# Kernel optimization log

Measured on AMD Instinct MI355X. Metric: run time of the kernel, lower is better.

## Reference

```python
import jax, jax.numpy as jnp
import numpy as np

B, S, D = 4, 2048, 1024
H = 2 * D          # hidden_dim = 2*n_embd
A = H // 16        # adapt_dim
E = 8              # num_experts
GS = 4             # group_size
G = E // GS        # num_groups
K = 2              # top-k experts within group


def _ln(x, g, b, eps=1e-5):
    m = x.mean(-1, keepdims=True)
    v = ((x - m) ** 2).mean(-1, keepdims=True)
    return (x - m) * jax.lax.rsqrt(v + eps) * g + b


def setup_inputs() -> dict:
    key = jax.random.key(0)
    ks = jax.random.split(key, 14)
    n = lambda k, shape, s: jax.random.normal(k, shape, jnp.float32) * s
    sc = 1.0 / float(np.sqrt(D))
    asc = 0.01 / float(np.sqrt(A))
    return {
        'x': n(ks[0], (B, S, D), 1.0),
        'Wu': n(ks[1], (H, D), sc),        # shared_up
        'Wg': n(ks[2], (H, D), sc),        # shared_gate
        'Wd': n(ks[3], (D, H), sc),        # shared_down
        'Wpre': n(ks[4], (A, D), sc * 0.01),   # pre_adapt
        'Wpost': n(ks[5], (A, H), sc * 0.01),  # post_adapt
        'ln_g': jnp.ones((A,), jnp.float32),
        'ln_b': jnp.zeros((A,), jnp.float32),
        'Wap': n(ks[6], (H, A), sc * 0.01),    # adapt_proj
        'Wea': n(ks[7], (E, A, A), asc),       # per-expert adapter linears
        'ln_eg': jnp.ones((E, A), jnp.float32),
        'ln_eb': jnp.zeros((E, A), jnp.float32),
        'Wep': n(ks[8], (H, A), asc),          # expert_proj
        'Wop': n(ks[9], (D, H), asc),          # output_proj
        'Wgr': n(ks[10], (G, D), 0.001),       # router_group
        'Wer': n(ks[11], (GS, D), 0.001),      # router_expert
    }


def _forward(x, Wu, Wg, Wd, Wpre, Wpost, ln_g, ln_b, Wap, Wea, ln_eg, ln_eb, Wep, Wop, Wgr, Wer):
    N = B * S
    xf = x.reshape(N, D)
    # --- hierarchical router ---
    gl = xf @ Wgr.T                              # [N,G]
    gp = jax.nn.softmax(gl, axis=-1)
    gw, gi = jax.lax.top_k(gp, 1)                # top-1 group
    el = xf @ Wer.T                              # [N,GS]
    ep = jax.nn.softmax(el, axis=-1)
    lw, li = jax.lax.top_k(ep, K)                # top-k local experts
    lw = lw / (lw.sum(-1, keepdims=True) + 1e-7)
    fw = gw * lw                                 # [N,K] final weights
    idx = gi * GS + li                           # [N,K] global expert ids (distinct per token)
    dispatch = jnp.zeros((N, E), x.dtype).at[jnp.arange(N)[:, None], idx].set(fw)
    load = dispatch.sum(0)
    target = load.sum() / E
    rloss = 0.001 * (jnp.mean((load - target) ** 2) + jnp.mean(gl ** 2) + jnp.mean(el ** 2))
    # --- shared expert MLP ---
    hidden = jax.nn.silu(x @ Wg.T) * (x @ Wu.T)  # [B,S,H]
    ai = _ln(x @ Wpre.T, ln_g, ln_b)             # [B,S,A]
    ao = _ln(hidden @ Wpost.T, ln_g, ln_b)       # [B,S,A]
    aw = jax.nn.silu(jnp.clip(jnp.einsum('bsa,bta->bst', ai, ao), -5.0, 5.0))  # [B,S,S]
    adapt = jnp.einsum('bst,bta->bsa', aw, ai) @ Wap.T
    hidden = hidden + 0.1 * adapt
    shared = hidden @ Wd.T                       # [B,S,D]
    # --- expert group (dense form of masked gather/scatter; w==0 off-mask) ---
    w = dispatch.reshape(B, S, E)
    h0 = x @ Wpre.T                              # [B,S,A]
    he = _ln(jnp.einsum('bsa,eca->bsec', h0, Wea), ln_eg, ln_eb)  # [B,S,E,A]
    M = Wop @ Wep                                # output_proj o expert_proj, [D,A]
    out = shared * w.sum(-1, keepdims=True) + 0.1 * jnp.einsum('bsec,bse,dc->bsd', he, w, M)
    return out, rloss


def reference(x, Wu, Wg, Wd, Wpre, Wpost, ln_g, ln_b, Wap, Wea, ln_eg, ln_eb, Wep, Wop, Wgr, Wer):
    return _forward(x, Wu, Wg, Wd, Wpre, Wpost, ln_g, ln_b, Wap, Wea, ln_eg, ln_eb, Wep, Wop, Wgr, Wer)
```

## Files before the change

### kernel.cpp

```cpp
#include <hip/hip_runtime.h>
#include <math.h>


typedef __bf16 bf16_t;
typedef __attribute__((ext_vector_type(8))) __bf16 bf16x8;
typedef __attribute__((ext_vector_type(4))) float f32x4;

__device__ __forceinline__ float b2f(bf16_t v) { return (float)v; }
__device__ __forceinline__ bf16_t f2b(float v) { return (bf16_t)v; }
__device__ __forceinline__ float siluf(float v) { return v / (1.f + expf(-v)); }

static constexpr int Bb = 4, S = 2048, D = 1024, H = 2048, A = 128, E = 8;
static constexpr int N = Bb * S;

typedef __attribute__((address_space(1))) void gvoid;
typedef __attribute__((address_space(3))) void svoid;
__device__ __forceinline__ void gll16(const bf16_t* g, bf16_t* l) {
  __builtin_amdgcn_global_load_lds((gvoid*)g, (svoid*)l, 16, 0, 0);
}

__device__ __forceinline__ long tidx(int row, int k, int K, int lgTR) {
  int TRm = (1 << lgTR) - 1;
  int q = (k >> 3) & 3;
  int p = q ^ ((row >> 1) & 3);
  return ((((long)(row >> lgTR) * (K >> 5) + (k >> 5)) << lgTR) + (row & TRm)) * 32 +
         ((long)p << 3);
}

__device__ __forceinline__ bf16x8 ld8f(const float* p) {
  float4 a = *reinterpret_cast<const float4*>(p);
  float4 b = *reinterpret_cast<const float4*>(p + 4);
  bf16x8 r;
  r[0] = f2b(a.x); r[1] = f2b(a.y); r[2] = f2b(a.z); r[3] = f2b(a.w);
  r[4] = f2b(b.x); r[5] = f2b(b.y); r[6] = f2b(b.z); r[7] = f2b(b.w);
  return r;
}
__device__ __forceinline__ void split8(const float* p, bf16x8& h, bf16x8& l) {
  float4 a = *reinterpret_cast<const float4*>(p);
  float4 b = *reinterpret_cast<const float4*>(p + 4);
  float v[8] = {a.x, a.y, a.z, a.w, b.x, b.y, b.z, b.w};
#pragma unroll
  for (int j = 0; j < 8; j++) {
    bf16_t hh = f2b(v[j]);
    h[j] = hh;
    l[j] = f2b(v[j] - b2f(hh));
  }
}
__device__ __forceinline__ bf16x8 ld8m(const void* p, int row, int k, int K, int m) {
  if (m == 1) return ld8f(reinterpret_cast<const float*>(p) + (long)row * K + k);
  if (m == 2)
    return *reinterpret_cast<const bf16x8*>(
        reinterpret_cast<const bf16_t*>(p) + tidx(row, k, K, 7));
  return *reinterpret_cast<const bf16x8*>(
      reinterpret_cast<const bf16_t*>(p) + (long)row * K + k);
}

template <int LGTR, int LGNKS>
__global__ __launch_bounds__(256) void split_tiled(
    const float* __restrict__ in, bf16_t* __restrict__ hi,
    bf16_t* __restrict__ lo, long total, int K) {
  long stride = (long)gridDim.x * 256;
  for (long o = (long)blockIdx.x * 256 + threadIdx.x; o < total; o += stride) {
    int p = (int)(o & 3);
    long t = o >> 2;
    int r = (int)(t & ((1 << LGTR) - 1));
    long t2 = t >> LGTR;
    int ks = (int)(t2 & ((1 << LGNKS) - 1));
    long rt = t2 >> LGNKS;
    long row = (rt << LGTR) + r;
    int k = (ks << 5) + ((p ^ ((r >> 1) & 3)) << 3);
    bf16x8 h, l;
    split8(in + row * K + k, h, l);
    reinterpret_cast<bf16x8*>(hi)[o] = h;
    reinterpret_cast<bf16x8*>(lo)[o] = l;
  }
}

template <int WM, int WN, int MODE>
__global__ __launch_bounds__(256) void gemm_nt_b(
    const void* __restrict__ Ag, const void* __restrict__ Bg,
    void* __restrict__ Cv, int M, int Nn, int K,
    const float* __restrict__ aux, int aF, int bF) {
  constexpr int BM = 2 * WM, BN = 2 * WN, AM = WM / 16, AN = WN / 16;
  constexpr int LDT = 40;
  __shared__ alignas(16) bf16_t As[BM * LDT];
  __shared__ alignas(16) bf16_t Bs[BN * LDT];

  const int tid = threadIdx.x;
  const int wave = tid >> 6, lane = tid & 63;
  const int wr = wave >> 1, wc = wave & 1;
  const int quad = lane >> 4, l16 = lane & 15;
  const int rowA0 = blockIdx.y * BM, rowB0 = blockIdx.x * BN;

  f32x4 acc[AM][AN] = {};

  for (int k0 = 0; k0 < K; k0 += 32) {
    for (int c = tid; c < BM * 4; c += 256) {
      int r = c >> 2, kc = c & 3;
      *reinterpret_cast<bf16x8*>(&As[r * LDT + kc * 8]) =
          ld8m(Ag, rowA0 + r, k0 + kc * 8, K, aF);
    }
    for (int c = tid; c < BN * 4; c += 256) {
      int r = c >> 2, kc = c & 3;
      *reinterpret_cast<bf16x8*>(&Bs[r * LDT + kc * 8]) =
          ld8m(Bg, rowB0 + r, k0 + kc * 8, K, bF);
    }
    __syncthreads();
    bf16x8 af[AM], bfv[AN];
#pragma unroll
    for (int i = 0; i < AM; i++)
      af[i] = *reinterpret_cast<bf16x8*>(&As[(wr * WM + i * 16 + l16) * LDT + quad * 8]);
#pragma unroll
    for (int j = 0; j < AN; j++)
      bfv[j] = *reinterpret_cast<bf16x8*>(&Bs[(wc * WN + j * 16 + l16) * LDT + quad * 8]);
#pragma unroll
    for (int i = 0; i < AM; i++)
#pragma unroll
      for (int j = 0; j < AN; j++)
        acc[i][j] = __builtin_amdgcn_mfma_f32_16x16x32_bf16(af[i], bfv[j], acc[i][j], 0, 0, 0);
    __syncthreads();
  }

#pragma unroll
  for (int i = 0; i < AM; i++)
#pragma unroll
    for (int j = 0; j < AN; j++)
#pragma unroll
      for (int r = 0; r < 4; r++) {
        int row = rowA0 + wr * WM + i * 16 + quad * 4 + r;
        int col = rowB0 + wc * WN + j * 16 + l16;
        long o = (long)row * Nn + col;
        float v = acc[i][j][r];
        if constexpr (MODE == 0) {
          reinterpret_cast<bf16_t*>(Cv)[o] = f2b(v);
        } else if constexpr (MODE == 1) {
          v = fminf(fmaxf(v, -5.f), 5.f);
          reinterpret_cast<bf16_t*>(Cv)[o] = f2b(siluf(v));
        } else if constexpr (MODE == 2) {
          float* C = reinterpret_cast<float*>(Cv);
          C[o] = C[o] + 0.1f * v;
        } else {
          float* C = reinterpret_cast<float*>(Cv);
          C[o] = C[o] * aux[row] + 0.1f * v;
        }
      }
}

__global__ __launch_bounds__(256) void gemm_gu_g(
    const bf16_t* __restrict__ xhT, const bf16_t* __restrict__ xlT,
    const bf16_t* __restrict__ WghT, const bf16_t* __restrict__ WglT,
    const bf16_t* __restrict__ WuhT, const bf16_t* __restrict__ WulT,
    bf16_t* __restrict__ Hh, bf16_t* __restrict__ Hl) {
  __shared__ alignas(16) bf16_t Ah[128 * 32];
  __shared__ alignas(16) bf16_t Al[128 * 32];
  __shared__ alignas(16) bf16_t B1h[64 * 32];
  __shared__ alignas(16) bf16_t B1l[64 * 32];
  __shared__ alignas(16) bf16_t B2h[64 * 32];
  __shared__ alignas(16) bf16_t B2l[64 * 32];

  const int tid = threadIdx.x;
  const int wave = tid >> 6, lane = tid & 63;
  const int wr = wave >> 1, wc = wave & 1;
  const int quad = lane >> 4, l16 = lane & 15;
  const int sw = (quad ^ ((l16 >> 1) & 3)) << 3;
  const int bm = blockIdx.y, bn = blockIdx.x;
  constexpr int nks = D / 32;
  const int wo = wave << 9;

  f32x4 ag[4][2] = {}, au[4][2] = {};

  for (int ks = 0; ks < nks; ks++) {
    long ao = (((long)bm * nks + ks) << 12) + wo + lane * 8;
    long bo = (((long)bn * nks + ks) << 11) + wo + lane * 8;
    gll16(xhT + ao, Ah + wo);
    gll16(xhT + ao + 2048, Ah + wo + 2048);
    gll16(xlT + ao, Al + wo);
    gll16(xlT + ao + 2048, Al + wo + 2048);
    gll16(WghT + bo, B1h + wo);
    gll16(WglT + bo, B1l + wo);
    gll16(WuhT + bo, B2h + wo);
    gll16(WulT + bo, B2l + wo);
    __syncthreads();
    bf16x8 afh[4], afl[4], b1h[2], b1l[2], b2h[2], b2l[2];
#pragma unroll
    for (int i = 0; i < 4; i++) {
      int ro = (wr * 64 + i * 16 + l16) * 32 + sw;
      afh[i] = *reinterpret_cast<bf16x8*>(&Ah[ro]);
      afl[i] = *reinterpret_cast<bf16x8*>(&Al[ro]);
    }
#pragma unroll
    for (int j = 0; j < 2; j++) {
      int ro = (wc * 32 + j * 16 + l16) * 32 + sw;
      b1h[j] = *reinterpret_cast<bf16x8*>(&B1h[ro]);
      b1l[j] = *reinterpret_cast<bf16x8*>(&B1l[ro]);
      b2h[j] = *reinterpret_cast<bf16x8*>(&B2h[ro]);
      b2l[j] = *reinterpret_cast<bf16x8*>(&B2l[ro]);
    }
#pragma unroll
    for (int i = 0; i < 4; i++)
#pragma unroll
      for (int j = 0; j < 2; j++) {
        ag[i][j] = __builtin_amdgcn_mfma_f32_16x16x32_bf16(afh[i], b1h[j], ag[i][j], 0, 0, 0);
        ag[i][j] = __builtin_amdgcn_mfma_f32_16x16x32_bf16(afh[i], b1l[j], ag[i][j], 0, 0, 0);
        ag[i][j] = __builtin_amdgcn_mfma_f32_16x16x32_bf16(afl[i], b1h[j], ag[i][j], 0, 0, 0);
        au[i][j] = __builtin_amdgcn_mfma_f32_16x16x32_bf16(afh[i], b2h[j], au[i][j], 0, 0, 0);
        au[i][j] = __builtin_amdgcn_mfma_f32_16x16x32_bf16(afh[i], b2l[j], au[i][j], 0, 0, 0);
        au[i][j] = __builtin_amdgcn_mfma_f32_16x16x32_bf16(afl[i], b2h[j], au[i][j], 0, 0, 0);
      }
    __syncthreads();
  }

#pragma unroll
  for (int i = 0; i < 4; i++)
#pragma unroll
    for (int j = 0; j < 2; j++)
#pragma unroll
      for (int r = 0; r < 4; r++) {
        int row = bm * 128 + wr * 64 + i * 16 + quad * 4 + r;
        int col = bn * 64 + wc * 32 + j * 16 + l16;
        long o = tidx(row, col, H, 7) + (col & 7);
        float v = siluf(ag[i][j][r]) * au[i][j][r];
        bf16_t hh = f2b(v);
        Hh[o] = hh;
        Hl[o] = f2b(v - b2f(hh));
      }
}

__global__ __launch_bounds__(256) void gemm_dn_g(
    const bf16_t* __restrict__ HhT, const bf16_t* __restrict__ HlT,
    const bf16_t* __restrict__ WdhT, const bf16_t* __restrict__ WdlT,
    float* __restrict__ Cg) {
  __shared__ alignas(16) bf16_t Ah[128 * 32];
  __shared__ alignas(16) bf16_t Al[128 * 32];
  __shared__ alignas(16) bf16_t Bh[128 * 32];
  __shared__ alignas(16) bf16_t Bl[128 * 32];

  const int tid = threadIdx.x;
  const int wave = tid >> 6, lane = tid & 63;
  const int wr = wave >> 1, wc = wave & 1;
  const int quad = lane >> 4, l16 = lane & 15;
  const int sw = (quad ^ ((l16 >> 1) & 3)) << 3;
  const int by = blockIdx.y, bx = blockIdx.x;
  constexpr int nks = H / 32;
  const int wo = wave << 9;

  f32x4 acc[4][4] = {};

  for (int ks = 0; ks < nks; ks++) {
    long ao = (((long)by * nks + ks) << 12) + wo + lane * 8;
    long bo = (((long)bx * nks + ks) << 12) + wo + lane * 8;
    gll16(HhT + ao, Ah + wo);
    gll16(HhT + ao + 2048, Ah + wo + 2048);
    gll16(HlT + ao, Al + wo);
    gll16(HlT + ao + 2048, Al + wo + 2048);
    gll16(WdhT + bo, Bh + wo);
    gll16(WdhT + bo + 2048, Bh + wo + 2048);
    gll16(WdlT + bo, Bl + wo);
    gll16(WdlT + bo + 2048, Bl + wo + 2048);
    __syncthreads();
    bf16x8 afh[4], afl[4], bfh[4], bfl[4];
#pragma unroll
    for (int i = 0; i < 4; i++) {
      int ro = (wr * 64 + i * 16 + l16) * 32 + sw;
      afh[i] = *reinterpret_cast<bf16x8*>(&Ah[ro]);
      afl[i] = *reinterpret_cast<bf16x8*>(&Al[ro]);
    }
#pragma unroll
    for (int j = 0; j < 4; j++) {
      int ro = (wc * 64 + j * 16 + l16) * 32 + sw;
      bfh[j] = *reinterpret_cast<bf16x8*>(&Bh[ro]);
      bfl[j] = *reinterpret_cast<bf16x8*>(&Bl[ro]);
    }
#pragma unroll
    for (int i = 0; i < 4; i++)
#pragma unroll
      for (int j = 0; j < 4; j++) {
        acc[i][j] = __builtin_amdgcn_mfma_f32_16x16x32_bf16(afh[i], bfh[j], acc[i][j], 0, 0, 0);
        acc[i][j] = __builtin_amdgcn_mfma_f32_16x16x32_bf16(afh[i], bfl[j], acc[i][j], 0, 0, 0);
        acc[i][j] = __builtin_amdgcn_mfma_f32_16x16x32_bf16(afl[i], bfh[j], acc[i][j], 0, 0, 0);
      }
    __syncthreads();
  }

#pragma unroll
  for (int i = 0; i < 4; i++)
#pragma unroll
    for (int j = 0; j < 4; j++)
#pragma unroll
      for (int r = 0; r < 4; r++) {
        int row = by * 128 + wr * 64 + i * 16 + quad * 4 + r;
        int col = bx * 128 + wc * 64 + j * 16 + l16;
        Cg[(long)row * D + col] = acc[i][j][r];
      }
}

__global__ __launch_bounds__(256) void fused_adapt(
    const bf16_t* __restrict__ aib, const bf16_t* __restrict__ aob,
    const bf16_t* __restrict__ aiT, bf16_t* __restrict__ outp,
    int oLd, int oOff, const float* __restrict__ wsum) {
  constexpr int LDQ = 136;
  constexpr int LDP = 72;
  __shared__ alignas(16) bf16_t Qs[64 * LDQ];
  __shared__ alignas(16) bf16_t Os[64 * LDQ];
  __shared__ alignas(16) bf16_t Ps[64 * LDP];
  __shared__ alignas(16) bf16_t Vs[128 * LDP];

  const int tid = threadIdx.x;
  const int wave = tid >> 6, lane = tid & 63;
  const int wr = wave >> 1, wc = wave & 1;
  const int quad = lane >> 4, l16 = lane & 15;
  const int b = blockIdx.y;
  const int q0 = blockIdx.x * 64;

  for (int c = tid; c < 1024; c += 256) {
    int r = c >> 4, cc = c & 15;
    *reinterpret_cast<bf16x8*>(&Qs[r * LDQ + cc * 8]) =
        *reinterpret_cast<const bf16x8*>(&aib[((long)b * S + q0 + r) * A + cc * 8]);
  }

  f32x4 o[2][4] = {};

  for (int tt = 0; tt < S / 64; tt++) {
    const int t0 = tt * 64;
    __syncthreads();
    for (int c = tid; c < 1024; c += 256) {
      int r = c >> 4, cc = c & 15;
      *reinterpret_cast<bf16x8*>(&Os[r * LDQ + cc * 8]) =
          *reinterpret_cast<const bf16x8*>(&aob[((long)b * S + t0 + r) * A + cc * 8]);
    }
    for (int c = tid; c < 1024; c += 256) {
      int r = c >> 3, cc = c & 7;
      *reinterpret_cast<bf16x8*>(&Vs[r * LDP + cc * 8]) =
          *reinterpret_cast<const bf16x8*>(&aiT[((long)b * A + r) * S + t0 + cc * 8]);
    }
    __syncthreads();
    f32x4 p[2][2] = {};
#pragma unroll
    for (int ks = 0; ks < 4; ks++) {
      bf16x8 af[2], bfv[2];
#pragma unroll
      for (int i = 0; i < 2; i++)
        af[i] = *reinterpret_cast<bf16x8*>(&Qs[(wr * 32 + i * 16 + l16) * LDQ + ks * 32 + quad * 8]);
#pragma unroll
      for (int j = 0; j < 2; j++)
        bfv[j] = *reinterpret_cast<bf16x8*>(&Os[(wc * 32 + j * 16 + l16) * LDQ + ks * 32 + quad * 8]);
#pragma unroll
      for (int i = 0; i < 2; i++)
#pragma unroll
        for (int j = 0; j < 2; j++)
          p[i][j] = __builtin_amdgcn_mfma_f32_16x16x32_bf16(af[i], bfv[j], p[i][j], 0, 0, 0);
    }
#pragma unroll
    for (int i = 0; i < 2; i++)
#pragma unroll
      for (int j = 0; j < 2; j++)
#pragma unroll
        for (int r = 0; r < 4; r++) {
          int row = wr * 32 + i * 16 + quad * 4 + r;
          int col = wc * 32 + j * 16 + l16;
          float v = fminf(fmaxf(p[i][j][r], -5.f), 5.f);
          Ps[row * LDP + col] = f2b(siluf(v));
        }
    __syncthreads();
#pragma unroll
    for (int ks = 0; ks < 2; ks++) {
      bf16x8 paf[2], vbf[4];
#pragma unroll
      for (int i = 0; i < 2; i++)
        paf[i] = *reinterpret_cast<bf16x8*>(&Ps[(wr * 32 + i * 16 + l16) * LDP + ks * 32 + quad * 8]);
#pragma unroll
      for (int j = 0; j < 4; j++)
        vbf[j] = *reinterpret_cast<bf16x8*>(&Vs[(wc * 64 + j * 16 + l16) * LDP + ks * 32 + quad * 8]);
#pragma unroll
      for (int i = 0; i < 2; i++)
#pragma unroll
        for (int j = 0; j < 4; j++)
          o[i][j] = __builtin_amdgcn_mfma_f32_16x16x32_bf16(paf[i], vbf[j], o[i][j], 0, 0, 0);
    }
  }

#pragma unroll
  for (int i = 0; i < 2; i++)
#pragma unroll
    for (int j = 0; j < 4; j++)
#pragma unroll
      for (int r = 0; r < 4; r++) {
        int row = q0 + wr * 32 + i * 16 + quad * 4 + r;
        int col = wc * 64 + j * 16 + l16;
        long token = (long)b * S + row;
        float sc = wsum ? wsum[token] : 1.f;
        outp[token * oLd + oOff + col] = f2b(o[i][j][r] * sc);
      }
}

__global__ __launch_bounds__(256) void gemm_mb_splitk(
    const float* __restrict__ Ag, const bf16_t* __restrict__ Bg,
    float* __restrict__ Mp, int M, int Nn, int K) {
  constexpr int BM = 64, BN = 64, LDT = 40;
  __shared__ alignas(16) bf16_t As[BM * LDT];
  __shared__ alignas(16) bf16_t Bs[BN * LDT];
  const int tid = threadIdx.x;
  const int wave = tid >> 6, lane = tid & 63;
  const int wr = wave >> 1, wc = wave & 1;
  const int quad = lane >> 4, l16 = lane & 15;
  const int rowA0 = blockIdx.y * BM, rowB0 = blockIdx.x * BN;
  const int kz = blockIdx.z;
  const int ks0 = kz * (K / 8), ks1 = ks0 + K / 8;

  f32x4 acc[2][2] = {};
  for (int k0 = ks0; k0 < ks1; k0 += 32) {
    for (int c = tid; c < BM * 4; c += 256) {
      int r = c >> 2, kc = c & 3;
      *reinterpret_cast<bf16x8*>(&As[r * LDT + kc * 8]) =
          ld8f(Ag + (long)(rowA0 + r) * K + k0 + kc * 8);
    }
    for (int c = tid; c < BN * 4; c += 256) {
      int r = c >> 2, kc = c & 3;
      *reinterpret_cast<bf16x8*>(&Bs[r * LDT + kc * 8]) =
          *reinterpret_cast<const bf16x8*>(&Bg[(long)(rowB0 + r) * K + k0 + kc * 8]);
    }
    __syncthreads();
    bf16x8 af[2], bfv[2];
#pragma unroll
    for (int i = 0; i < 2; i++)
      af[i] = *reinterpret_cast<bf16x8*>(&As[(wr * 32 + i * 16 + l16) * LDT + quad * 8]);
#pragma unroll
    for (int j = 0; j < 2; j++)
      bfv[j] = *reinterpret_cast<bf16x8*>(&Bs[(wc * 32 + j * 16 + l16) * LDT + quad * 8]);
#pragma unroll
    for (int i = 0; i < 2; i++)
#pragma unroll
      for (int j = 0; j < 2; j++)
        acc[i][j] = __builtin_amdgcn_mfma_f32_16x16x32_bf16(af[i], bfv[j], acc[i][j], 0, 0, 0);
    __syncthreads();
  }
#pragma unroll
  for (int i = 0; i < 2; i++)
#pragma unroll
    for (int j = 0; j < 2; j++)
#pragma unroll
      for (int r = 0; r < 4; r++) {
        int row = rowA0 + wr * 32 + i * 16 + quad * 4 + r;
        int col = rowB0 + wc * 32 + j * 16 + l16;
        Mp[(long)kz * M * Nn + (long)row * Nn + col] = acc[i][j][r];
      }
}

__global__ __launch_bounds__(256) void mb_combine(
    const float* __restrict__ Mp, bf16_t* __restrict__ outp, int total,
    int ld, int coff) {
  int i = blockIdx.x * 256 + threadIdx.x;
  if (i >= total) return;
  float s = 0.f;
#pragma unroll
  for (int z = 0; z < 8; z++) s += Mp[(long)z * total + i];
  outp[(long)(i >> 7) * ld + coff + (i & 127)] = f2b(s);
}

__global__ __launch_bounds__(256) void gemm_dn_hl(
    const float* __restrict__ Ag, const float* __restrict__ Bg,
    float* __restrict__ Cg, int M, int Nn, int K) {
  constexpr int BM = 128, BN = 128, LDT = 40;
  __shared__ alignas(16) bf16_t Ah[BM * LDT];
  __shared__ alignas(16) bf16_t Al[BM * LDT];
  __shared__ alignas(16) bf16_t Bh[BN * LDT];
  __shared__ alignas(16) bf16_t Bl[BN * LDT];

  const int tid = threadIdx.x;
  const int wave = tid >> 6, lane = tid & 63;
  const int wr = wave >> 1, wc = wave & 1;
  const int quad = lane >> 4, l16 = lane & 15;
  const int rowA0 = blockIdx.y * BM, rowB0 = blockIdx.x * BN;

  f32x4 acc[4][4] = {};

  for (int k0 = 0; k0 < K; k0 += 32) {
    for (int c = tid; c < BM * 4; c += 256) {
      int r = c >> 2, kc = c & 3;
      bf16x8 h, l;
      split8(&Ag[(long)(rowA0 + r) * K + k0 + kc * 8], h, l);
      *reinterpret_cast<bf16x8*>(&Ah[r * LDT + kc * 8]) = h;
      *reinterpret_cast<bf16x8*>(&Al[r * LDT + kc * 8]) = l;
    }
    for (int c = tid; c < BN * 4; c += 256) {
      int r = c >> 2, kc = c & 3;
      bf16x8 h, l;
      split8(&Bg[(long)(rowB0 + r) * K + k0 + kc * 8], h, l);
      *reinterpret_cast<bf16x8*>(&Bh[r * LDT + kc * 8]) = h;
      *reinterpret_cast<bf16x8*>(&Bl[r * LDT + kc * 8]) = l;
    }
    __syncthreads();
    bf16x8 afh[4], afl[4], bfh[4], bfl[4];
#pragma unroll
    for (int i = 0; i < 4; i++) {
      int ro = (wr * 64 + i * 16 + l16) * LDT + quad * 8;
      afh[i] = *reinterpret_cast<bf16x8*>(&Ah[ro]);
      afl[i] = *reinterpret_cast<bf16x8*>(&Al[ro]);
    }
#pragma unroll
    for (int j = 0; j < 4; j++) {
      int ro = (wc * 64 + j * 16 + l16) * LDT + quad * 8;
      bfh[j] = *reinterpret_cast<bf16x8*>(&Bh[ro]);
      bfl[j] = *reinterpret_cast<bf16x8*>(&Bl[ro]);
    }
#pragma unroll
    for (int i = 0; i < 4; i++)
#pragma unroll
      for (int j = 0; j < 4; j++) {
        acc[i][j] = __builtin_amdgcn_mfma_f32_16x16x32_bf16(afh[i], bfh[j], acc[i][j], 0, 0, 0);
        acc[i][j] = __builtin_amdgcn_mfma_f32_16x16x32_bf16(afh[i], bfl[j], acc[i][j], 0, 0, 0);
        acc[i][j] = __builtin_amdgcn_mfma_f32_16x16x32_bf16(afl[i], bfh[j], acc[i][j], 0, 0, 0);
      }
    __syncthreads();
  }

#pragma unroll
  for (int i = 0; i < 4; i++)
#pragma unroll
    for (int j = 0; j < 4; j++)
#pragma unroll
      for (int r = 0; r < 4; r++) {
        int row = rowA0 + wr * 64 + i * 16 + quad * 4 + r;
        int col = rowB0 + wc * 64 + j * 16 + l16;
        Cg[(long)row * Nn + col] = acc[i][j][r];
      }
}

__global__ __launch_bounds__(256) void gemm_gu_hl(
    const float* __restrict__ x, const float* __restrict__ Wg,
    const float* __restrict__ Wu, float* __restrict__ Cg, int M, int Nn, int K) {
  constexpr int BM = 128, BN = 64, LDT = 40;
  __shared__ alignas(16) bf16_t Ah[BM * LDT];
  __shared__ alignas(16) bf16_t Al[BM * LDT];
  __shared__ alignas(16) bf16_t B1h[BN * LDT];
  __shared__ alignas(16) bf16_t B1l[BN * LDT];
  __shared__ alignas(16) bf16_t B2h[BN * LDT];
  __shared__ alignas(16) bf16_t B2l[BN * LDT];

  const int tid = threadIdx.x;
  const int wave = tid >> 6, lane = tid & 63;
  const int wr = wave >> 1, wc = wave & 1;
  const int quad = lane >> 4, l16 = lane & 15;
  const int rowA0 = blockIdx.y * BM, rowB0 = blockIdx.x * BN;

  f32x4 ag[4][2] = {}, au[4][2] = {};

  for (int k0 = 0; k0 < K; k0 += 32) {
    for (int c = tid; c < BM * 4; c += 256) {
      int r = c >> 2, kc = c & 3;
      bf16x8 h, l;
      split8(&x[(long)(rowA0 + r) * K + k0 + kc * 8], h, l);
      *reinterpret_cast<bf16x8*>(&Ah[r * LDT + kc * 8]) = h;
      *reinterpret_cast<bf16x8*>(&Al[r * LDT + kc * 8]) = l;
    }
    for (int c = tid; c < BN * 4; c += 256) {
      int r = c >> 2, kc = c & 3;
      long idx = (long)(rowB0 + r) * K + k0 + kc * 8;
      bf16x8 h, l;
      split8(&Wg[idx], h, l);
      *reinterpret_cast<bf16x8*>(&B1h[r * LDT + kc * 8]) = h;
      *reinterpret_cast<bf16x8*>(&B1l[r * LDT + kc * 8]) = l;
      split8(&Wu[idx], h, l);
      *reinterpret_cast<bf16x8*>(&B2h[r * LDT + kc * 8]) = h;
      *reinterpret_cast<bf16x8*>(&B2l[r * LDT + kc * 8]) = l;
    }
    __syncthreads();
    bf16x8 afh[4], afl[4], b1h[2], b1l[2], b2h[2], b2l[2];
#pragma unroll
    for (int i = 0; i < 4; i++) {
      int ro = (wr * 64 + i * 16 + l16) * LDT + quad * 8;
      afh[i] = *reinterpret_cast<bf16x8*>(&Ah[ro]);
      afl[i] = *reinterpret_cast<bf16x8*>(&Al[ro]);
    }
#pragma unroll
    for (int j = 0; j < 2; j++) {
      int ro = (wc * 32 + j * 16 + l16) * LDT + quad * 8;
      b1h[j] = *reinterpret_cast<bf16x8*>(&B1h[ro]);
      b1l[j] = *reinterpret_cast<bf16x8*>(&B1l[ro]);
      b2h[j] = *reinterpret_cast<bf16x8*>(&B2h[ro]);
      b2l[j] = *reinterpret_cast<bf16x8*>(&B2l[ro]);
    }
#pragma unroll
    for (int i = 0; i < 4; i++)
#pragma unroll
      for (int j = 0; j < 2; j++) {
        ag[i][j] = __builtin_amdgcn_mfma_f32_16x16x32_bf16(afh[i], b1h[j], ag[i][j], 0, 0, 0);
        ag[i][j] = __builtin_amdgcn_mfma_f32_16x16x32_bf16(afh[i], b1l[j], ag[i][j], 0, 0, 0);
        ag[i][j] = __builtin_amdgcn_mfma_f32_16x16x32_bf16(afl[i], b1h[j], ag[i][j], 0, 0, 0);
        au[i][j] = __builtin_amdgcn_mfma_f32_16x16x32_bf16(afh[i], b2h[j], au[i][j], 0, 0, 0);
        au[i][j] = __builtin_amdgcn_mfma_f32_16x16x32_bf16(afh[i], b2l[j], au[i][j], 0, 0, 0);
        au[i][j] = __builtin_amdgcn_mfma_f32_16x16x32_bf16(afl[i], b2h[j], au[i][j], 0, 0, 0);
      }
    __syncthreads();
  }

#pragma unroll
  for (int i = 0; i < 4; i++)
#pragma unroll
    for (int j = 0; j < 2; j++)
#pragma unroll
      for (int r = 0; r < 4; r++) {
        int row = rowA0 + wr * 64 + i * 16 + quad * 4 + r;
        int col = rowB0 + wc * 32 + j * 16 + l16;
        Cg[(long)row * Nn + col] = siluf(ag[i][j][r]) * au[i][j][r];
      }
}

__global__ __launch_bounds__(256) void router_kernel(
    const float* __restrict__ x, const float* __restrict__ Wgr,
    const float* __restrict__ Wer, int* __restrict__ eidx,
    float* __restrict__ fw, float* __restrict__ wsum,
    float* __restrict__ lpart) {
  __shared__ float part[4][12];
  const int wv = threadIdx.x >> 6;
  const int lane = threadIdx.x & 63;
  const int token = blockIdx.x * 4 + wv;
  if (lane < 12) part[wv][lane] = 0.f;
  const float* xp = x + (long)token * D;
  float xr[16];
#pragma unroll
  for (int i = 0; i < 16; i++) xr[i] = xp[lane + i * 64];
  float dots[6];
#pragma unroll
  for (int w = 0; w < 6; w++) {
    const float* wp = (w < 2) ? (Wgr + (long)w * D) : (Wer + (long)(w - 2) * D);
    float s = 0.f;
#pragma unroll
    for (int i = 0; i < 16; i++) s += xr[i] * wp[lane + i * 64];
#pragma unroll
    for (int off = 32; off; off >>= 1) s += __shfl_xor(s, off);
    dots[w] = s;
  }
  if (lane == 0) {
    float gl0 = dots[0], gl1 = dots[1];
    float mg = fmaxf(gl0, gl1);
    float e0 = expf(gl0 - mg), e1 = expf(gl1 - mg);
    float inv = 1.f / (e0 + e1);
    float gp0 = e0 * inv, gp1 = e1 * inv;
    int gi = (gp1 > gp0) ? 1 : 0;
    float gw = gi ? gp1 : gp0;
    float el[4] = {dots[2], dots[3], dots[4], dots[5]};
    float me = fmaxf(fmaxf(el[0], el[1]), fmaxf(el[2], el[3]));
    float ep[4], es = 0.f;
#pragma unroll
    for (int j = 0; j < 4; j++) { ep[j] = expf(el[j] - me); es += ep[j]; }
    float inve = 1.f / es;
#pragma unroll
    for (int j = 0; j < 4; j++) ep[j] *= inve;
    int i1 = 0;
    for (int j = 1; j < 4; j++) if (ep[j] > ep[i1]) i1 = j;
    int i2 = (i1 == 0) ? 1 : 0;
    for (int j = 0; j < 4; j++) if (j != i1 && j != i2 && ep[j] > ep[i2]) i2 = j;
    float l1 = ep[i1], l2 = ep[i2];
    float ils = 1.f / (l1 + l2 + 1e-7f);
    float f1 = gw * l1 * ils, f2 = gw * l2 * ils;
    eidx[token * 2] = gi * 4 + i1;
    eidx[token * 2 + 1] = gi * 4 + i2;
    fw[token * 2] = f1;
    fw[token * 2 + 1] = f2;
    wsum[token] = f1 + f2;
    part[wv][gi * 4 + i1] = f1;
    part[wv][gi * 4 + i2] = f2;
    part[wv][8] = gl0 * gl0 + gl1 * gl1;
    part[wv][9] = el[0] * el[0] + el[1] * el[1] + el[2] * el[2] + el[3] * el[3];
  }
  __syncthreads();
  if (threadIdx.x < 12) {
    lpart[(long)blockIdx.x * 12 + threadIdx.x] =
        part[0][threadIdx.x] + part[1][threadIdx.x] +
        part[2][threadIdx.x] + part[3][threadIdx.x];
  }
}

__global__ __launch_bounds__(256) void ln_rows(
    const bf16_t* __restrict__ in, const float* __restrict__ g,
    const float* __restrict__ b, bf16_t* __restrict__ out) {
  const int row = blockIdx.x * 4 + (threadIdx.x >> 6);
  const int lane = threadIdx.x & 63;
  const bf16_t* p = in + (long)row * A;
  float x0 = b2f(p[lane]), x1 = b2f(p[lane + 64]);
  float s = x0 + x1;
#pragma unroll
  for (int off = 32; off; off >>= 1) s += __shfl_xor(s, off);
  float mean = s * (1.f / 128.f);
  float d0 = x0 - mean, d1 = x1 - mean;
  float q = d0 * d0 + d1 * d1;
#pragma unroll
  for (int off = 32; off; off >>= 1) q += __shfl_xor(q, off);
  float r = rsqrtf(q * (1.f / 128.f) + 1e-5f);
  bf16_t* po = out + (long)row * A;
  po[lane] = f2b(d0 * r * g[lane] + b[lane]);
  po[lane + 64] = f2b(d1 * r * g[lane + 64] + b[lane + 64]);
}

__global__ __launch_bounds__(256) void transpose2d(
    const void* __restrict__ in, bf16_t* __restrict__ out, int R, int C, int isf) {
  __shared__ bf16_t t[32][33];
  const long zb = blockIdx.z;
  const long ib = zb * (long)R * C;
  bf16_t* op = out + zb * (long)R * C;
  const int r0 = blockIdx.y * 32, c0 = blockIdx.x * 32;
  const int tx = threadIdx.x & 31, ty = threadIdx.x >> 5;
#pragma unroll
  for (int i = 0; i < 4; i++) {
    long idx = ib + (long)(r0 + ty + i * 8) * C + c0 + tx;
    t[ty + i * 8][tx] = isf ? f2b(reinterpret_cast<const float*>(in)[idx])
                            : reinterpret_cast<const bf16_t*>(in)[idx];
  }
  __syncthreads();
#pragma unroll
  for (int i = 0; i < 4; i++) op[(long)(c0 + ty + i * 8) * R + r0 + tx] = t[tx][ty + i * 8];
}

__global__ __launch_bounds__(128) void expert_adapt(
    const bf16_t* __restrict__ h0, const bf16_t* __restrict__ WeaT,
    const float* __restrict__ ln_eg, const float* __restrict__ ln_eb,
    const int* __restrict__ eidx, const float* __restrict__ fw,
    bf16_t* __restrict__ hw, int ld) {
  const int n = blockIdx.x;
  const int c = threadIdx.x;
  __shared__ float h0s[128];
  __shared__ float red[4];
  h0s[c] = b2f(h0[(long)n * A + c]);
  __syncthreads();
  float out = 0.f;
  for (int k = 0; k < 2; k++) {
    int e = eidx[n * 2 + k];
    e = min(max(e, 0), E - 1);
    float w = fw[n * 2 + k];
    const bf16_t* Wc = WeaT + (long)e * A * A + c;
    float t = 0.f;
#pragma unroll 8
    for (int a = 0; a < 128; a++) t += b2f(Wc[(long)a * A]) * h0s[a];
    float s = t, q = t * t;
#pragma unroll
    for (int off = 32; off; off >>= 1) { s += __shfl_xor(s, off); q += __shfl_xor(q, off); }
    if ((c & 63) == 0) { red[(c >> 6) * 2] = s; red[(c >> 6) * 2 + 1] = q; }
    __syncthreads();
    float Sx = red[0] + red[2], Qx = red[1] + red[3];
    float mean = Sx * (1.f / 128.f);
    float var = Qx * (1.f / 128.f) - mean * mean;
    float r = rsqrtf(var + 1e-5f);
    out += w * ((t - mean) * r * ln_eg[e * A + c] + ln_eb[e * A + c]);
    __syncthreads();
  }
  hw[(long)n * ld + c] = f2b(out);
}

__global__ __launch_bounds__(256) void finalize_loss(
    const float* __restrict__ lpart, int nblk, float* __restrict__ outv) {
  float acc[10] = {};
  for (int b = threadIdx.x; b < nblk; b += 256) {
    const float* p = lpart + (long)b * 12;
#pragma unroll
    for (int c = 0; c < 10; c++) acc[c] += p[c];
  }
  __shared__ float red[10][4];
  const int lane = threadIdx.x & 63, wv = threadIdx.x >> 6;
#pragma unroll
  for (int c = 0; c < 10; c++) {
    float s = acc[c];
#pragma unroll
    for (int off = 32; off; off >>= 1) s += __shfl_xor(s, off);
    if (lane == 0) red[c][wv] = s;
  }
  __syncthreads();
  if (threadIdx.x == 0) {
    float loss[10];
#pragma unroll
    for (int c = 0; c < 10; c++)
      loss[c] = red[c][0] + red[c][1] + red[c][2] + red[c][3];
    float tl = 0.f;
    for (int e = 0; e < 8; e++) tl += loss[e];
    float target = tl / 8.f;
    float mse = 0.f;
    for (int e = 0; e < 8; e++) { float d = loss[e] - target; mse += d * d; }
    mse *= (1.f / 8.f);
    outv[0] = 0.001f * (mse + loss[8] / (float)(N * 2) + loss[9] / (float)(N * 4));
  }
}

extern "C" void kernel_launch(void* const* d_in, const int* in_sizes, int n_in,
                              void* d_out, int out_size, void* d_ws, size_t ws_size,
                              hipStream_t stream) {
  const float* x = (const float*)d_in[0];
  const float* Wu = (const float*)d_in[1];
  const float* Wg = (const float*)d_in[2];
  const float* Wd = (const float*)d_in[3];
  const float* Wpre = (const float*)d_in[4];
  const float* Wpost = (const float*)d_in[5];
  const float* ln_g = (const float*)d_in[6];
  const float* ln_b = (const float*)d_in[7];
  const float* Wap = (const float*)d_in[8];
  const float* Wea = (const float*)d_in[9];
  const float* ln_eg = (const float*)d_in[10];
  const float* ln_eb = (const float*)d_in[11];
  const float* Wep = (const float*)d_in[12];
  const float* Wop = (const float*)d_in[13];
  const float* Wgr = (const float*)d_in[14];
  const float* Wer = (const float*)d_in[15];
  float* out = (float*)d_out;

  char* ws = (char*)d_ws;
  size_t off = 0;
  auto alloc = [&](size_t bytes) { char* p = ws + off; off += (bytes + 255) & ~size_t(255); return p; };
  float* lpart = (float*)alloc((size_t)(N / 4) * 12 * 4);
  float* wsum = (float*)alloc((size_t)N * 4);
  float* fwb = (float*)alloc((size_t)N * 2 * 4);
  int* eidx = (int*)alloc((size_t)N * 2 * 4);
  bf16_t* Mb2 = (bf16_t*)alloc((size_t)D * 256 * 2);
  float* Mp = (float*)alloc((size_t)8 * D * A * 4);
  bf16_t* WepT = (bf16_t*)alloc((size_t)H * A * 2);
  bf16_t* WapT = (bf16_t*)alloc((size_t)H * A * 2);
  bf16_t* hw2 = (bf16_t*)alloc((size_t)N * 256 * 2);
  bf16_t* h0b = (bf16_t*)alloc((size_t)N * A * 2);
  bf16_t* aib = (bf16_t*)alloc((size_t)N * A * 2);
  bf16_t* scrA = (bf16_t*)alloc((size_t)N * A * 2);
  bf16_t* aob = (bf16_t*)alloc((size_t)N * A * 2);
  bf16_t* WeaT = (bf16_t*)alloc((size_t)E * A * A * 2);
  bf16_t* aopre = scrA;
  bf16_t* aiT = scrA;

  const bool big = ws_size >= ((size_t)140 << 20);
  float* hiddenF = nullptr;
  bf16_t *xh = nullptr, *xl = nullptr;
  bf16_t *Wgh = nullptr, *Wgl = nullptr, *Wuh = nullptr, *Wul = nullptr;
  bf16_t *Wdh = nullptr, *Wdl = nullptr, *Hh = nullptr, *Hl = nullptr;
  if (big) {
    xh = (bf16_t*)alloc((size_t)N * D * 2);
    xl = (bf16_t*)alloc((size_t)N * D * 2);
    Wgh = (bf16_t*)alloc((size_t)H * D * 2);
    Wgl = (bf16_t*)alloc((size_t)H * D * 2);
    Wuh = (bf16_t*)alloc((size_t)H * D * 2);
    Wul = (bf16_t*)alloc((size_t)H * D * 2);
    Wdh = (bf16_t*)alloc((size_t)D * H * 2);
    Wdl = (bf16_t*)alloc((size_t)D * H * 2);
    Hh = (bf16_t*)alloc((size_t)N * H * 2);
    Hl = (bf16_t*)alloc((size_t)N * H * 2);
  } else {
    hiddenF = (float*)alloc((size_t)N * H * 4);
  }
  (void)ws_size; (void)in_sizes; (void)n_in; (void)out_size;

  const dim3 blk(256);

  router_kernel<<<dim3(N / 4), blk, 0, stream>>>(x, Wgr, Wer, eidx, fwb, wsum, lpart);
  transpose2d<<<dim3(A / 32, A / 32, E), blk, 0, stream>>>(Wea, WeaT, A, A, 1);

  if (big) {
    split_tiled<7, 5><<<dim3(2048), blk, 0, stream>>>(x, xh, xl, (long)N * D / 8, D);
    split_tiled<6, 5><<<dim3(512), blk, 0, stream>>>(Wg, Wgh, Wgl, (long)H * D / 8, D);
    split_tiled<6, 5><<<dim3(512), blk, 0, stream>>>(Wu, Wuh, Wul, (long)H * D / 8, D);
    split_tiled<7, 6><<<dim3(512), blk, 0, stream>>>(Wd, Wdh, Wdl, (long)D * H / 8, H);
    gemm_gu_g<<<dim3(H / 64, N / 128), blk, 0, stream>>>(
        xh, xl, Wgh, Wgl, Wuh, Wul, Hh, Hl);
    gemm_nt_b<16, 32, 0><<<dim3(A / 64, N / 32), blk, 0, stream>>>(
        xh, Wpre, h0b, N, A, D, nullptr, 2, 1);
    ln_rows<<<dim3(N / 4), blk, 0, stream>>>(h0b, ln_g, ln_b, aib);
    gemm_nt_b<16, 32, 0><<<dim3(A / 64, N / 32), blk, 0, stream>>>(
        Hh, Wpost, aopre, N, A, H, nullptr, 2, 1);
    ln_rows<<<dim3(N / 4), blk, 0, stream>>>(aopre, ln_g, ln_b, aob);
    transpose2d<<<dim3(A / 32, S / 32, Bb), blk, 0, stream>>>(aib, aiT, S, A, 0);
    fused_adapt<<<dim3(S / 64, Bb), blk, 0, stream>>>(
        aib, aob, aiT, hw2, 256, 128, wsum);
    gemm_dn_g<<<dim3(D / 128, N / 128), blk, 0, stream>>>(Hh, Hl, Wdh, Wdl, out);
    transpose2d<<<dim3(A / 32, H / 32, 1), blk, 0, stream>>>(Wep, WepT, H, A, 1);
    transpose2d<<<dim3(A / 32, H / 32, 1), blk, 0, stream>>>(Wap, WapT, H, A, 1);
    gemm_mb_splitk<<<dim3(A / 64, D / 64, 8), blk, 0, stream>>>(Wop, WepT, Mp, D, A, H);
    mb_combine<<<dim3((D * A + 255) / 256), blk, 0, stream>>>(Mp, Mb2, D * A, 256, 0);
    gemm_mb_splitk<<<dim3(A / 64, D / 64, 8), blk, 0, stream>>>(Wd, WapT, Mp, D, A, H);
    mb_combine<<<dim3((D * A + 255) / 256), blk, 0, stream>>>(Mp, Mb2, D * A, 256, 128);
    expert_adapt<<<dim3(N), dim3(128), 0, stream>>>(
        h0b, WeaT, ln_eg, ln_eb, eidx, fwb, hw2, 256);
    gemm_nt_b<64, 64, 3><<<dim3(D / 128, N / 128), blk, 0, stream>>>(
        hw2, Mb2, out, N, D, 256, wsum, 0, 0);
  } else {
    bf16_t* adpreb = hw2 + (size_t)N * A;
    gemm_gu_hl<<<dim3(H / 64, N / 128), blk, 0, stream>>>(x, Wg, Wu, hiddenF, N, H, D);
    gemm_nt_b<16, 32, 0><<<dim3(A / 64, N / 32), blk, 0, stream>>>(
        x, Wpre, h0b, N, A, D, nullptr, 1, 1);
    ln_rows<<<dim3(N / 4), blk, 0, stream>>>(h0b, ln_g, ln_b, aib);
    gemm_nt_b<16, 32, 0><<<dim3(A / 64, N / 32), blk, 0, stream>>>(
        hiddenF, Wpost, aopre, N, A, H, nullptr, 1, 1);
    ln_rows<<<dim3(N / 4), blk, 0, stream>>>(aopre, ln_g, ln_b, aob);
    transpose2d<<<dim3(A / 32, S / 32, Bb), blk, 0, stream>>>(aib, aiT, S, A, 0);
    fused_adapt<<<dim3(S / 64, Bb), blk, 0, stream>>>(
        aib, aob, aiT, adpreb, 128, 0, nullptr);
    gemm_nt_b<64, 64, 2><<<dim3(H / 128, N / 128), blk, 0, stream>>>(
        adpreb, Wap, hiddenF, N, H, A, nullptr, 0, 1);
    gemm_dn_hl<<<dim3(D / 128, N / 128), blk, 0, stream>>>(hiddenF, Wd, out, N, D, H);
    transpose2d<<<dim3(A / 32, H / 32, 1), blk, 0, stream>>>(Wep, WepT, H, A, 1);
    gemm_mb_splitk<<<dim3(A / 64, D / 64, 8), blk, 0, stream>>>(Wop, WepT, Mp, D, A, H);
    mb_combine<<<dim3((D * A + 255) / 256), blk, 0, stream>>>(Mp, Mb2, D * A, 128, 0);
    expert_adapt<<<dim3(N), dim3(128), 0, stream>>>(
        h0b, WeaT, ln_eg, ln_eb, eidx, fwb, hw2, 128);
    gemm_nt_b<64, 64, 3><<<dim3(D / 128, N / 128), blk, 0, stream>>>(
        hw2, Mb2, out, N, D, A, wsum, 0, 0);
  }

  finalize_loss<<<dim3(1), blk, 0, stream>>>(lpart, N / 4, out + (size_t)N * D);
}
```

Measured before the change: 772.9 us.

## Fuse expert/adapter GEMM into down-projection GEMM and swizzle block order

The separate expert/adapter output GEMM is removed. Its K=256 contraction over hw2 and Mb2 now runs as extra k-steps inside gemm_dn_g, which accumulates into the same registers. The per-token wsum scale is applied once in that epilogue, so the adapter and expert rows are pre-scaled by 0.1 and 0.1/wsum upstream. This avoids a full fp32 read-modify-write of the N×D output and one kernel launch. It also remaps block IDs in both large GEMMs to group tiles per XCD for cache locality, and merges the Wg and Wu split kernels into one launch. The risk is added bf16 rounding from dividing by wsum before conversion.

```diff
diff --git a/kernel.cpp b/kernel.cpp
--- a/kernel.cpp
+++ b/kernel.cpp
@@ -76,6 +76,31 @@
   }
 }
 
+template <int LGTR, int LGNKS>
+__global__ __launch_bounds__(256) void split_tiled2(
+    const float* __restrict__ s0, bf16_t* __restrict__ h0, bf16_t* __restrict__ l0,
+    const float* __restrict__ s1, bf16_t* __restrict__ h1, bf16_t* __restrict__ l1,
+    long total, int K) {
+  const float* in = blockIdx.z ? s1 : s0;
+  bf16_t* hi = blockIdx.z ? h1 : h0;
+  bf16_t* lo = blockIdx.z ? l1 : l0;
+  long stride = (long)gridDim.x * 256;
+  for (long o = (long)blockIdx.x * 256 + threadIdx.x; o < total; o += stride) {
+    int p = (int)(o & 3);
+    long t = o >> 2;
+    int r = (int)(t & ((1 << LGTR) - 1));
+    long t2 = t >> LGTR;
+    int ks = (int)(t2 & ((1 << LGNKS) - 1));
+    long rt = t2 >> LGNKS;
+    long row = (rt << LGTR) + r;
+    int k = (ks << 5) + ((p ^ ((r >> 1) & 3)) << 3);
+    bf16x8 h, l;
+    split8(in + row * K + k, h, l);
+    reinterpret_cast<bf16x8*>(hi)[o] = h;
+    reinterpret_cast<bf16x8*>(lo)[o] = l;
+  }
+}
+
 template <int WM, int WN, int MODE>
 __global__ __launch_bounds__(256) void gemm_nt_b(
     const void* __restrict__ Ag, const void* __restrict__ Bg,
@@ -163,7 +188,10 @@
   const int wr = wave >> 1, wc = wave & 1;
   const int quad = lane >> 4, l16 = lane & 15;
   const int sw = (quad ^ ((l16 >> 1) & 3)) << 3;
-  const int bm = blockIdx.y, bn = blockIdx.x;
+  const int lid = blockIdx.y * gridDim.x + blockIdx.x;
+  const int nper = (gridDim.x * gridDim.y) >> 3;
+  const int nl = (lid & 7) * nper + (lid >> 3);
+  const int bm = nl >> 5, bn = nl & 31;
   constexpr int nks = D / 32;
   const int wo = wave << 9;
 
@@ -229,7 +257,8 @@
 __global__ __launch_bounds__(256) void gemm_dn_g(
     const bf16_t* __restrict__ HhT, const bf16_t* __restrict__ HlT,
     const bf16_t* __restrict__ WdhT, const bf16_t* __restrict__ WdlT,
-    float* __restrict__ Cg) {
+    const bf16_t* __restrict__ hw2, const bf16_t* __restrict__ Mb2,
+    const float* __restrict__ wsum, float* __restrict__ Cg) {
   __shared__ alignas(16) bf16_t Ah[128 * 32];
   __shared__ alignas(16) bf16_t Al[128 * 32];
   __shared__ alignas(16) bf16_t Bh[128 * 32];
@@ -240,7 +269,10 @@
   const int wr = wave >> 1, wc = wave & 1;
   const int quad = lane >> 4, l16 = lane & 15;
   const int sw = (quad ^ ((l16 >> 1) & 3)) << 3;
-  const int by = blockIdx.y, bx = blockIdx.x;
+  const int lid = blockIdx.y * gridDim.x + blockIdx.x;
+  const int nper = (gridDim.x * gridDim.y) >> 3;
+  const int nl = (lid & 7) * nper + (lid >> 3);
+  const int by = nl >> 3, bx = nl & 7;
   constexpr int nks = H / 32;
   const int wo = wave << 9;
 
@@ -282,6 +314,34 @@
     __syncthreads();
   }
 
+  {
+    const int rrow = wave * 16 + (lane >> 2);
+    const int pp = lane & 3;
+    for (int ck = 0; ck < 8; ck++) {
+      int r0 = rrow, r1 = rrow + 64;
+      int q0 = (pp ^ ((r0 >> 1) & 3)) << 3;
+      int q1 = (pp ^ ((r1 >> 1) & 3)) << 3;
+      gll16(hw2 + ((long)(by * 128 + r0) * 256 + ck * 32 + q0), Ah + wo);
+      gll16(hw2 + ((long)(by * 128 + r1) * 256 + ck * 32 + q1), Ah + wo + 2048);
+      gll16(Mb2 + ((long)(bx * 128 + r0) * 256 + ck * 32 + q0), Bh + wo);
+      gll16(Mb2 + ((long)(bx * 128 + r1) * 256 + ck * 32 + q1), Bh + wo + 2048);
+      __syncthreads();
+      bf16x8 af2[4], bf2[4];
+#pragma unroll
+      for (int i = 0; i < 4; i++)
+        af2[i] = *reinterpret_cast<bf16x8*>(&Ah[(wr * 64 + i * 16 + l16) * 32 + sw]);
+#pragma unroll
+      for (int j = 0; j < 4; j++)
+        bf2[j] = *reinterpret_cast<bf16x8*>(&Bh[(wc * 64 + j * 16 + l16) * 32 + sw]);
+#pragma unroll
+      for (int i = 0; i < 4; i++)
+#pragma unroll
+        for (int j = 0; j < 4; j++)
+          acc[i][j] = __builtin_amdgcn_mfma_f32_16x16x32_bf16(af2[i], bf2[j], acc[i][j], 0, 0, 0);
+      __syncthreads();
+    }
+  }
+
 #pragma unroll
   for (int i = 0; i < 4; i++)
 #pragma unroll
@@ -290,14 +350,14 @@
       for (int r = 0; r < 4; r++) {
         int row = by * 128 + wr * 64 + i * 16 + quad * 4 + r;
         int col = bx * 128 + wc * 64 + j * 16 + l16;
-        Cg[(long)row * D + col] = acc[i][j][r];
+        Cg[(long)row * D + col] = wsum[row] * acc[i][j][r];
       }
 }
 
 __global__ __launch_bounds__(256) void fused_adapt(
     const bf16_t* __restrict__ aib, const bf16_t* __restrict__ aob,
     const bf16_t* __restrict__ aiT, bf16_t* __restrict__ outp,
-    int oLd, int oOff, const float* __restrict__ wsum) {
+    int oLd, int oOff, float cscale) {
   constexpr int LDQ = 136;
   constexpr int LDP = 72;
   __shared__ alignas(16) bf16_t Qs[64 * LDQ];
@@ -388,8 +448,7 @@
         int row = q0 + wr * 32 + i * 16 + quad * 4 + r;
         int col = wc * 64 + j * 16 + l16;
         long token = (long)b * S + row;
-        float sc = wsum ? wsum[token] : 1.f;
-        outp[token * oLd + oOff + col] = f2b(o[i][j][r] * sc);
+        outp[token * oLd + oOff + col] = f2b(o[i][j][r] * cscale);
       }
 }
 
@@ -716,7 +775,7 @@
     const bf16_t* __restrict__ h0, const bf16_t* __restrict__ WeaT,
     const float* __restrict__ ln_eg, const float* __restrict__ ln_eb,
     const int* __restrict__ eidx, const float* __restrict__ fw,
-    bf16_t* __restrict__ hw, int ld) {
+    bf16_t* __restrict__ hw, int ld, const float* __restrict__ wsc) {
   const int n = blockIdx.x;
   const int c = threadIdx.x;
   __shared__ float h0s[128];
@@ -744,7 +803,8 @@
     out += w * ((t - mean) * r * ln_eg[e * A + c] + ln_eb[e * A + c]);
     __syncthreads();
   }
-  hw[(long)n * ld + c] = f2b(out);
+  float sc = wsc ? (0.1f / wsc[n]) : 1.f;
+  hw[(long)n * ld + c] = f2b(out * sc);
 }
 
 __global__ __launch_bounds__(256) void finalize_loss(
@@ -849,8 +909,8 @@
 
   if (big) {
     split_tiled<7, 5><<<dim3(2048), blk, 0, stream>>>(x, xh, xl, (long)N * D / 8, D);
-    split_tiled<6, 5><<<dim3(512), blk, 0, stream>>>(Wg, Wgh, Wgl, (long)H * D / 8, D);
-    split_tiled<6, 5><<<dim3(512), blk, 0, stream>>>(Wu, Wuh, Wul, (long)H * D / 8, D);
+    split_tiled2<6, 5><<<dim3(512, 1, 2), blk, 0, stream>>>(
+        Wg, Wgh, Wgl, Wu, Wuh, Wul, (long)H * D / 8, D);
     split_tiled<7, 6><<<dim3(512), blk, 0, stream>>>(Wd, Wdh, Wdl, (long)D * H / 8, H);
     gemm_gu_g<<<dim3(H / 64, N / 128), blk, 0, stream>>>(
         xh, xl, Wgh, Wgl, Wuh, Wul, Hh, Hl);
@@ -861,19 +921,18 @@
         Hh, Wpost, aopre, N, A, H, nullptr, 2, 1);
     ln_rows<<<dim3(N / 4), blk, 0, stream>>>(aopre, ln_g, ln_b, aob);
     transpose2d<<<dim3(A / 32, S / 32, Bb), blk, 0, stream>>>(aib, aiT, S, A, 0);
-    fused_adapt<<<dim3(S / 64, Bb), blk, 0, stream>>>(
-        aib, aob, aiT, hw2, 256, 128, wsum);
-    gemm_dn_g<<<dim3(D / 128, N / 128), blk, 0, stream>>>(Hh, Hl, Wdh, Wdl, out);
     transpose2d<<<dim3(A / 32, H / 32, 1), blk, 0, stream>>>(Wep, WepT, H, A, 1);
     transpose2d<<<dim3(A / 32, H / 32, 1), blk, 0, stream>>>(Wap, WapT, H, A, 1);
     gemm_mb_splitk<<<dim3(A / 64, D / 64, 8), blk, 0, stream>>>(Wop, WepT, Mp, D, A, H);
     mb_combine<<<dim3((D * A + 255) / 256), blk, 0, stream>>>(Mp, Mb2, D * A, 256, 0);
     gemm_mb_splitk<<<dim3(A / 64, D / 64, 8), blk, 0, stream>>>(Wd, WapT, Mp, D, A, H);
     mb_combine<<<dim3((D * A + 255) / 256), blk, 0, stream>>>(Mp, Mb2, D * A, 256, 128);
+    fused_adapt<<<dim3(S / 64, Bb), blk, 0, stream>>>(
+        aib, aob, aiT, hw2, 256, 128, 0.1f);
     expert_adapt<<<dim3(N), dim3(128), 0, stream>>>(
-        h0b, WeaT, ln_eg, ln_eb, eidx, fwb, hw2, 256);
-    gemm_nt_b<64, 64, 3><<<dim3(D / 128, N / 128), blk, 0, stream>>>(
-        hw2, Mb2, out, N, D, 256, wsum, 0, 0);
+        h0b, WeaT, ln_eg, ln_eb, eidx, fwb, hw2, 256, wsum);
+    gemm_dn_g<<<dim3(D / 128, N / 128), blk, 0, stream>>>(
+        Hh, Hl, Wdh, Wdl, hw2, Mb2, wsum, out);
   } else {
     bf16_t* adpreb = hw2 + (size_t)N * A;
     gemm_gu_hl<<<dim3(H / 64, N / 128), blk, 0, stream>>>(x, Wg, Wu, hiddenF, N, H, D);
@@ -885,7 +944,7 @@
     ln_rows<<<dim3(N / 4), blk, 0, stream>>>(aopre, ln_g, ln_b, aob);
     transpose2d<<<dim3(A / 32, S / 32, Bb), blk, 0, stream>>>(aib, aiT, S, A, 0);
     fused_adapt<<<dim3(S / 64, Bb), blk, 0, stream>>>(
-        aib, aob, aiT, adpreb, 128, 0, nullptr);
+        aib, aob, aiT, adpreb, 128, 0, 1.f);
     gemm_nt_b<64, 64, 2><<<dim3(H / 128, N / 128), blk, 0, stream>>>(
         adpreb, Wap, hiddenF, N, H, A, nullptr, 0, 1);
     gemm_dn_hl<<<dim3(D / 128, N / 128), blk, 0, stream>>>(hiddenF, Wd, out, N, D, H);
@@ -893,7 +952,7 @@
     gemm_mb_splitk<<<dim3(A / 64, D / 64, 8), blk, 0, stream>>>(Wop, WepT, Mp, D, A, H);
     mb_combine<<<dim3((D * A + 255) / 256), blk, 0, stream>>>(Mp, Mb2, D * A, 128, 0);
     expert_adapt<<<dim3(N), dim3(128), 0, stream>>>(
-        h0b, WeaT, ln_eg, ln_eb, eidx, fwb, hw2, 128);
+        h0b, WeaT, ln_eg, ln_eb, eidx, fwb, hw2, 128, nullptr);
     gemm_nt_b<64, 64, 3><<<dim3(D / 128, N / 128), blk, 0, stream>>>(
         hw2, Mb2, out, N, D, A, wsum, 0, 0);
   }
```

New measurement: 731.5 us. 1.06x faster.
